# Kernel optimization log

Measured on AMD Instinct MI355X. Metric: run time of the kernel, lower is better.

## Reference

```python
import jax, jax.numpy as jnp
import numpy as np

B, K, D = 16384, 64, 128


def setup_inputs() -> dict:
    key = jax.random.key(0)
    kx, kc = jax.random.split(key)
    x = jax.random.normal(kx, (B, D), dtype=jnp.float32)
    centers = jax.random.uniform(kc, (K, D), dtype=jnp.float32)  # torch.rand init
    return {"x": x, "centers": centers}


def reference(x, centers):
    batch, dim = x.shape
    k = centers.shape[0]
    # pairwise squared distances, same math as sum((x - c)^2)
    diff = x[:, None, :] - centers[None, :, :]          # [B, K, D]
    dist_sq = jnp.sum(diff * diff, axis=-1)             # [B, K]
    expo = -0.5 * dist_sq
    # safe softmax over clusters (identical to max-subtracted exp/sum)
    resp = jax.nn.softmax(expo, axis=-1)                # [B, K]
    log_resp = jnp.log(jnp.clip(resp, 1e-8))
    # hard assignment and per-cluster statistics
    assign = jnp.argmin(dist_sq, axis=-1)               # [B] int
    onehot = jax.nn.one_hot(assign, k, dtype=x.dtype)   # [B, K]
    cluster_weight = jnp.sum(onehot, axis=0)            # [K]
    emp_total = jnp.einsum('nk,nd->kd', onehot, x)      # [K, D]
    emp_mean = emp_total / (cluster_weight[:, None] + 1e-7)
    # masked centered samples: onehot[n,k]*(x_n - mean_k) is nonzero only at k=assign(n)
    xm = x - emp_mean[assign]                           # [B, D]
    covar_total = jnp.einsum('nk,nd,ne->kde', onehot, xm, xm)  # [K, D, D]
    covar = covar_total / (cluster_weight[:, None, None] + 1e-7)
    eye = jnp.eye(dim, dtype=x.dtype)
    covar_diag = covar * eye
    covar_off = covar * (1.0 - eye)
    diag_dist_sq = jnp.sum((covar_diag - eye) ** 2, axis=(1, 2))  # [K]
    off_dist_sq = jnp.sum(covar_off ** 2, axis=(1, 2))            # [K]
    mean_dist_sq = jnp.sum((emp_mean - centers) ** 2, axis=1)     # [K]
    mean_mse = jnp.sum(cluster_weight * mean_dist_sq) / (batch * dim)
    covar_mse = jnp.sum(
        cluster_weight * diag_dist_sq / (batch * dim)
        + cluster_weight * off_dist_sq / (batch * dim * (dim - 1.0))
    )
    return log_resp, mean_mse, covar_mse
```

## Files before the change

### kernel.cpp

```cpp
#include <hip/hip_runtime.h>

#define BB 16384
#define KK 64
#define DD 128
#define SEG 128
#define MAXITEMS 192
#define NRB 4
#define RSLAB 4096
#define RBLKS (KK * NRB)

typedef __attribute__((ext_vector_type(8))) short bf16x8;
typedef __attribute__((ext_vector_type(4))) float f32x4;

__device__ __forceinline__ unsigned int packbf2(float a, float b) {
    unsigned ua = __float_as_uint(a);
    unsigned ub = __float_as_uint(b);
    ua = (ua + 0x7FFFu + ((ua >> 16) & 1u)) >> 16;
    ub = (ub + 0x7FFFu + ((ub >> 16) & 1u)) >> 16;
    return ua | (ub << 16);
}

__device__ __forceinline__ unsigned bf16rne(float f) {
    unsigned u = __float_as_uint(f);
    return (u + 0x7FFFu + ((u >> 16) & 1u)) >> 16;
}
__device__ __forceinline__ float bf16tof(unsigned h) {
    return __uint_as_float(h << 16);
}
__device__ __forceinline__ void split4(float4 v, uint2& hi, uint2& lo) {
    unsigned hx = bf16rne(v.x), hy = bf16rne(v.y);
    unsigned hz = bf16rne(v.z), hw = bf16rne(v.w);
    hi.x = hx | (hy << 16); hi.y = hz | (hw << 16);
    unsigned lx = bf16rne(v.x - bf16tof(hx)), ly = bf16rne(v.y - bf16tof(hy));
    unsigned lz = bf16rne(v.z - bf16tof(hz)), lw = bf16rne(v.w - bf16tof(hw));
    lo.x = lx | (ly << 16); lo.y = lz | (lw << 16);
}

__global__ __launch_bounds__(256) void k_rows(
    const float* __restrict__ x, const float* __restrict__ centers,
    float* __restrict__ log_resp, int* __restrict__ assign,
    int* __restrict__ bhist, int* __restrict__ counter)
{
    __shared__ unsigned int XH[64][68], XLo[64][68];
    __shared__ unsigned int CH[64][68], CLo[64][68];
    __shared__ float cn2_s[KK];
    __shared__ int   lh[KK];

    const int tid = threadIdx.x;
    const int row0 = blockIdx.x * 64;

    if (blockIdx.x == 0 && tid == 0) *counter = 0;
    if (tid < KK) lh[tid] = 0;

    for (int g = tid; g < 64 * 32; g += 256) {
        int r = g >> 5, c4g = g & 31;
        float4 v = ((const float4*)(x + (size_t)(row0 + r) * DD))[c4g];
        uint2 hi, lo; split4(v, hi, lo);
        *(uint2*)&XH[r][c4g * 2] = hi;
        *(uint2*)&XLo[r][c4g * 2] = lo;
    }
    for (int g = tid; g < 64 * 32; g += 256) {
        int k = g >> 5, c4g = g & 31;
        float4 v = ((const float4*)(centers + (size_t)k * DD))[c4g];
        uint2 hi, lo; split4(v, hi, lo);
        *(uint2*)&CH[k][c4g * 2] = hi;
        *(uint2*)&CLo[k][c4g * 2] = lo;
    }
    if (tid < KK) {
        float s = 0.f;
        const float4* cp = (const float4*)(centers + (size_t)tid * DD);
        for (int c4g = 0; c4g < 32; ++c4g) {
            float4 v = cp[c4g];
            s = fmaf(v.x, v.x, s); s = fmaf(v.y, v.y, s);
            s = fmaf(v.z, v.z, s); s = fmaf(v.w, v.w, s);
        }
        cn2_s[tid] = s;
    }
    __syncthreads();

    const int w = tid >> 6, lane = tid & 63;
    const int c4 = lane & 15, q = lane >> 4;

    f32x4 acc[4];
    #pragma unroll
    for (int nt = 0; nt < 4; ++nt) acc[nt] = (f32x4){0.f, 0.f, 0.f, 0.f};

    #pragma unroll
    for (int c = 0; c < 4; ++c) {
        const int ku = c * 16 + q * 4;
        bf16x8 ah = *(const bf16x8*)&XH[w * 16 + c4][ku];
        bf16x8 al = *(const bf16x8*)&XLo[w * 16 + c4][ku];
        #pragma unroll
        for (int nt = 0; nt < 4; ++nt) {
            bf16x8 bh = *(const bf16x8*)&CH[nt * 16 + c4][ku];
            bf16x8 bl = *(const bf16x8*)&CLo[nt * 16 + c4][ku];
            acc[nt] = __builtin_amdgcn_mfma_f32_16x16x32_bf16(ah, bh, acc[nt], 0, 0, 0);
            acc[nt] = __builtin_amdgcn_mfma_f32_16x16x32_bf16(ah, bl, acc[nt], 0, 0, 0);
            acc[nt] = __builtin_amdgcn_mfma_f32_16x16x32_bf16(al, bh, acc[nt], 0, 0, 0);
        }
    }

    float cn[4];
    #pragma unroll
    for (int nt = 0; nt < 4; ++nt) cn[nt] = 0.5f * cn2_s[nt * 16 + c4];

    #pragma unroll
    for (int j = 0; j < 4; ++j) {
        const int row = row0 + w * 16 + q * 4 + j;
        float v0 = acc[0][j] - cn[0];
        float v1 = acc[1][j] - cn[1];
        float v2 = acc[2][j] - cn[2];
        float v3 = acc[3][j] - cn[3];
        float m = v0; int idx = c4;
        if (v1 > m) { m = v1; idx = 16 + c4; }
        if (v2 > m) { m = v2; idx = 32 + c4; }
        if (v3 > m) { m = v3; idx = 48 + c4; }
        #pragma unroll
        for (int off = 1; off < 16; off <<= 1) {
            float ov = __shfl_xor(m, off);
            int   oi = __shfl_xor(idx, off);
            if (ov > m || (ov == m && oi < idx)) { m = ov; idx = oi; }
        }
        float s = expf(v0 - m) + expf(v1 - m) + expf(v2 - m) + expf(v3 - m);
        #pragma unroll
        for (int off = 1; off < 16; off <<= 1) s += __shfl_xor(s, off);
        float ls = logf(s);
        log_resp[(size_t)row * KK +  0 + c4] = fmaxf(v0 - m - ls, -18.4206807f);
        log_resp[(size_t)row * KK + 16 + c4] = fmaxf(v1 - m - ls, -18.4206807f);
        log_resp[(size_t)row * KK + 32 + c4] = fmaxf(v2 - m - ls, -18.4206807f);
        log_resp[(size_t)row * KK + 48 + c4] = fmaxf(v3 - m - ls, -18.4206807f);
        if (c4 == 0) {
            assign[row] = idx;
            atomicAdd(&lh[idx], 1);
        }
    }
    __syncthreads();
    if (tid < KK) bhist[blockIdx.x * KK + tid] = lh[tid];
}

__global__ __launch_bounds__(256) void k_scat(
    const int* __restrict__ assign, const int* __restrict__ bhist,
    int* __restrict__ sorted, float* __restrict__ cw,
    int4* __restrict__ items, int* __restrict__ item_count,
    int* __restrict__ ist, int* __restrict__ ien)
{
    __shared__ int ph_tot[4][KK], ph_pre[4][KK];
    __shared__ int cnt_s[KK], pre_s[KK], base_s[KK], cur_s[KK];
    __shared__ int iof[KK + 1];

    const int tid = threadIdx.x;
    const int b = blockIdx.x;
    const int t = tid & 63, q = tid >> 6;

    int tot = 0, pre = 0;
    const int bb0 = q * 64;
    for (int bb = bb0; bb < bb0 + 64; ++bb) {
        int v = bhist[bb * KK + t];
        tot += v;
        if (bb < b) pre += v;
    }
    ph_tot[q][t] = tot; ph_pre[q][t] = pre;
    __syncthreads();

    if (tid < KK) {
        cnt_s[tid] = ph_tot[0][tid] + ph_tot[1][tid] + ph_tot[2][tid] + ph_tot[3][tid];
        pre_s[tid] = ph_pre[0][tid] + ph_pre[1][tid] + ph_pre[2][tid] + ph_pre[3][tid];
        cur_s[tid] = 0;
    }
    __syncthreads();
    if (tid == 0) {
        int base = 0;
        for (int k = 0; k < KK; ++k) { base_s[k] = base; base += cnt_s[k]; }
    }
    __syncthreads();

    if (tid < 64) {
        int r = b * 64 + tid;
        int a = assign[r];
        int p = base_s[a] + pre_s[a] + atomicAdd(&cur_s[a], 1);
        sorted[p] = r;
    }

    if (b == 0) {
        if (tid < KK) cw[tid] = (float)cnt_s[tid];
        if (tid == 0) {
            int ic = 0;
            for (int k = 0; k < KK; ++k) {
                iof[k] = ic;
                ic += (cnt_s[k] + SEG - 1) / SEG;
            }
            iof[KK] = ic;
            *item_count = ic;
        }
        __syncthreads();
        if (tid < KK) {
            const int k = tid, c = cnt_s[k], io = iof[k];
            ist[k] = io;
            ien[k] = iof[k + 1];
            int j = 0;
            for (int s = 0; s < c; s += SEG, ++j) {
                int4 it; it.x = k; it.y = base_s[k] + s;
                it.z = min(SEG, c - s); it.w = 0;
                items[io + j] = it;
            }
        }
    }
}

__global__ __launch_bounds__(256) void k_seg(
    const float* __restrict__ x, const int* __restrict__ sorted,
    const int4* __restrict__ items, const int* __restrict__ item_count,
    float* __restrict__ part, float* __restrict__ emp_part)
{
    if ((int)blockIdx.x >= *item_count) return;
    int4 it = items[blockIdx.x];
    const int gstart = it.y, len = it.z;

    __shared__ int rows_s[128];
    __shared__ unsigned int XT[DD][68];

    const int tid = threadIdx.x;
    const int w = tid >> 6, lane = tid & 63;
    const int c4 = lane & 15, q = lane >> 4;

    f32x4 acc[2][8];
    #pragma unroll
    for (int h = 0; h < 2; ++h)
        #pragma unroll
        for (int nt = 0; nt < 8; ++nt)
            acc[h][nt] = (f32x4){0.f, 0.f, 0.f, 0.f};
    float colsum = 0.f;

    for (int half = 0; half < 2; ++half) {
        const int hoff = half * 128;
        const int hlen = min(128, len - hoff);
        if (hlen <= 0) break;

        __syncthreads();
        if (tid < hlen) rows_s[tid] = sorted[gstart + hoff + tid];
        __syncthreads();

        {
            const int r0 = 2 * lane, r1 = 2 * lane + 1;
            const int d0 = w * 32;
            const float* p0 = x + (size_t)rows_s[r0 < hlen ? r0 : 0] * DD + d0;
            const float* p1 = x + (size_t)rows_s[r1 < hlen ? r1 : 0] * DD + d0;
            #pragma unroll
            for (int i = 0; i < 8; ++i) {
                float4 a = make_float4(0.f, 0.f, 0.f, 0.f);
                float4 b = make_float4(0.f, 0.f, 0.f, 0.f);
                if (r0 < hlen) a = *(const float4*)(p0 + 4 * i);
                if (r1 < hlen) b = *(const float4*)(p1 + 4 * i);
                XT[d0 + 4 * i + 0][lane] = packbf2(a.x, b.x);
                XT[d0 + 4 * i + 1][lane] = packbf2(a.y, b.y);
                XT[d0 + 4 * i + 2][lane] = packbf2(a.z, b.z);
                XT[d0 + 4 * i + 3][lane] = packbf2(a.w, b.w);
            }
        }
        __syncthreads();

        if (tid < DD) {
            float s = 0.f;
            #pragma unroll
            for (int j4 = 0; j4 < 16; ++j4) {
                uint4 v = *(const uint4*)&XT[tid][j4 * 4];
                s += __uint_as_float(v.x << 16) + __uint_as_float(v.x & 0xFFFF0000u);
                s += __uint_as_float(v.y << 16) + __uint_as_float(v.y & 0xFFFF0000u);
                s += __uint_as_float(v.z << 16) + __uint_as_float(v.z & 0xFFFF0000u);
                s += __uint_as_float(v.w << 16) + __uint_as_float(v.w & 0xFFFF0000u);
            }
            colsum += s;
        }

        #pragma unroll
        for (int c = 0; c < 4; ++c) {
            const int ku = c * 16 + q * 4;
            bf16x8 a0 = *(const bf16x8*)&XT[(2 * w + 0) * 16 + c4][ku];
            bf16x8 a1 = *(const bf16x8*)&XT[(2 * w + 1) * 16 + c4][ku];
            #pragma unroll
            for (int nt = 0; nt < 8; ++nt) {
                bf16x8 b = *(const bf16x8*)&XT[nt * 16 + c4][ku];
                acc[0][nt] = __builtin_amdgcn_mfma_f32_16x16x32_bf16(a0, b, acc[0][nt], 0, 0, 0);
                acc[1][nt] = __builtin_amdgcn_mfma_f32_16x16x32_bf16(a1, b, acc[1][nt], 0, 0, 0);
            }
        }
    }

    if (tid < DD) emp_part[blockIdx.x * DD + tid] = colsum;

    float* pb = part + (size_t)blockIdx.x * (DD * DD);
    #pragma unroll
    for (int h = 0; h < 2; ++h) {
        const int m0 = (2 * w + h) * 16 + q * 4;
        #pragma unroll
        for (int nt = 0; nt < 8; ++nt) {
            const int n = nt * 16 + c4;
            pb[(m0 + 0) * DD + n] = acc[h][nt].x;
            pb[(m0 + 1) * DD + n] = acc[h][nt].y;
            pb[(m0 + 2) * DD + n] = acc[h][nt].z;
            pb[(m0 + 3) * DD + n] = acc[h][nt].w;
        }
    }
}

__global__ __launch_bounds__(256) void k_redfinal(
    const float* __restrict__ part, const float* __restrict__ emp_part,
    const float* __restrict__ cw, const float* __restrict__ centers,
    const int* __restrict__ ist, const int* __restrict__ ien,
    float2* __restrict__ spart, int* __restrict__ counter,
    float* __restrict__ outscalars)
{
    const int k = blockIdx.x >> 2;
    const int p = blockIdx.x & 3;
    const int i0 = ist[k], i1 = ien[k];
    const int tid = threadIdx.x;
    const int w = tid >> 6, lane = tid & 63;
    const float wgt = cw[k];
    const float inv = 1.0f / (wgt + 1e-7f);

    __shared__ float mu_s[DD], emp_s[DD];
    __shared__ float emp2[2][DD];
    __shared__ float red[4][RSLAB];

    {
        const int dh = tid & 127, hf = tid >> 7;
        float e0 = 0.f, e1 = 0.f;
        int it = i0 + hf;
        for (; it + 2 < i1; it += 4) {
            e0 += emp_part[it * DD + dh];
            e1 += emp_part[(it + 2) * DD + dh];
        }
        if (it < i1) e0 += emp_part[it * DD + dh];
        emp2[hf][dh] = e0 + e1;
    }
    __syncthreads();
    if (tid < DD) {
        float e = emp2[0][tid] + emp2[1][tid];
        emp_s[tid] = e;
        mu_s[tid] = e * inv;
    }

    float4 acc[16];
    #pragma unroll
    for (int c = 0; c < 16; ++c) acc[c] = make_float4(0.f, 0.f, 0.f, 0.f);

    const int base = p * RSLAB;
    for (int it = i0 + w; it < i1; it += 4) {
        const float* pb = part + (size_t)it * (DD * DD) + base;
        #pragma unroll
        for (int c = 0; c < 16; ++c) {
            float4 v = *(const float4*)&pb[c * 256 + lane * 4];
            acc[c].x += v.x; acc[c].y += v.y; acc[c].z += v.z; acc[c].w += v.w;
        }
    }
    #pragma unroll
    for (int c = 0; c < 16; ++c)
        *(float4*)&red[w][c * 256 + lane * 4] = acc[c];
    __syncthreads();

    float ds = 0.f, os = 0.f, mm = 0.f;
    #pragma unroll
    for (int jj = 0; jj < 16; ++jj) {
        int el = jj * 256 + tid;
        float sx = red[0][el] + red[1][el] + red[2][el] + red[3][el];
        int gel = base + el;
        int d = gel >> 7, e = gel & 127;
        float ctv = sx - mu_s[d] * emp_s[e] - emp_s[d] * mu_s[e]
                  + wgt * mu_s[d] * mu_s[e];
        float v = ctv * inv;
        if (d == e) { float t = v - 1.f; ds += t * t; }
        else        { os += v * v; }
    }
    if (p == 0 && tid < DD) {
        float t = mu_s[tid] - centers[k * DD + tid];
        mm = t * t;
    }

    #pragma unroll
    for (int off = 32; off > 0; off >>= 1) {
        ds += __shfl_down(ds, off);
        os += __shfl_down(os, off);
        mm += __shfl_down(mm, off);
    }
    __shared__ float rds[4], ros[4], rmm[4];
    __shared__ int is_last;
    if (lane == 0) { rds[w] = ds; ros[w] = os; rmm[w] = mm; }
    __syncthreads();
    if (tid == 0) {
        float DS = rds[0] + rds[1] + rds[2] + rds[3];
        float OS = ros[0] + ros[1] + ros[2] + ros[3];
        float MM = rmm[0] + rmm[1] + rmm[2] + rmm[3];
        const float bd = (float)BB * (float)DD;
        float2 mine;
        mine.x = wgt * MM / bd;
        mine.y = wgt * DS / bd + wgt * OS / (bd * (float)(DD - 1));
        spart[blockIdx.x] = mine;
        __threadfence();
        int old = atomicAdd(counter, 1);
        is_last = (old == RBLKS - 1);
    }
    __syncthreads();
    if (is_last) {
        __threadfence();
        float2 v = (tid < RBLKS) ? spart[tid] : make_float2(0.f, 0.f);
        float a = v.x, b = v.y;
        #pragma unroll
        for (int off = 32; off > 0; off >>= 1) {
            a += __shfl_down(a, off);
            b += __shfl_down(b, off);
        }
        __shared__ float ra[4], rb[4];
        if (lane == 0) { ra[w] = a; rb[w] = b; }
        __syncthreads();
        if (tid == 0) {
            outscalars[0] = ra[0] + ra[1] + ra[2] + ra[3];
            outscalars[1] = rb[0] + rb[1] + rb[2] + rb[3];
        }
    }
}

extern "C" void kernel_launch(void* const* d_in, const int* in_sizes, int n_in,
                              void* d_out, int out_size, void* d_ws, size_t ws_size,
                              hipStream_t stream) {
    const float* x = (const float*)d_in[0];
    const float* centers = (const float*)d_in[1];
    float* out = (float*)d_out;
    float* outscalars = out + (size_t)BB * KK;

    char* ws = (char*)d_ws;
    size_t off = 0;
    float*  part     = (float*)(ws + off); off += (size_t)MAXITEMS * DD * DD * 4;
    float*  emp_part = (float*)(ws + off); off += (size_t)MAXITEMS * DD * 4;
    int*    sorted   = (int*)  (ws + off); off += BB * 4;
    int*    assign   = (int*)  (ws + off); off += BB * 4;
    int*    bhist    = (int*)  (ws + off); off += 256 * KK * 4;
    int4*   items    = (int4*) (ws + off); off += 256 * 16;
    float*  cw       = (float*)(ws + off); off += 256;
    int*    itemcnt  = (int*)  (ws + off); off += 256;
    int*    ist      = (int*)  (ws + off); off += 256;
    int*    ien      = (int*)  (ws + off); off += 256;
    float2* spart    = (float2*)(ws + off); off += RBLKS * 8;
    int*    counter  = (int*)  (ws + off); off += 256;

    k_rows    <<<256, 256, 0, stream>>>(x, centers, out, assign, bhist, counter);
    k_scat    <<<256, 256, 0, stream>>>(assign, bhist, sorted, cw, items,
                                        itemcnt, ist, ien);
    k_seg     <<<MAXITEMS, 256, 0, stream>>>(x, sorted, items, itemcnt,
                                             part, emp_part);
    k_redfinal<<<RBLKS, 256, 0, stream>>>(part, emp_part, cw, centers, ist, ien,
                                          spart, counter, outscalars);
}
```

Before: 111.4 us.

## Widen segment blocks to eight waves and split reduction into more slabs

Each segment GEMM block now runs 512 threads in a single pass over its at-most-128 rows. Every wave computes one 16-row stripe of the 128x128 outer product instead of two, and the dead second half-loop is removed. The per-cluster reduction is split into 8 slabs of 2048 elements instead of 4 of 4096. That halves per-block shared memory and registers and doubles the number of reduction blocks, with the final scalar reduce adjusted to read 512 partials. The aim is more parallelism and occupancy in the two bandwidth-heavy stages, at the cost of more blocks and a little extra per-block setup.

New measurement: 115.1 us. 1.03x slower.

```diff
diff --git a/kernel.cpp b/kernel.cpp
--- a/kernel.cpp
+++ b/kernel.cpp
@@ -5,8 +5,8 @@
 #define DD 128
 #define SEG 128
 #define MAXITEMS 192
-#define NRB 4
-#define RSLAB 4096
+#define NRB 8
+#define RSLAB 2048
 #define RBLKS (KK * NRB)
 
 typedef __attribute__((ext_vector_type(8))) short bf16x8;
@@ -207,7 +207,7 @@
     }
 }
 
-__global__ __launch_bounds__(256) void k_seg(
+__global__ __launch_bounds__(512) void k_seg(
     const float* __restrict__ x, const int* __restrict__ sorted,
     const int4* __restrict__ items, const int* __restrict__ item_count,
     float* __restrict__ part, float* __restrict__ emp_part)
@@ -223,83 +223,65 @@
     const int w = tid >> 6, lane = tid & 63;
     const int c4 = lane & 15, q = lane >> 4;
 
-    f32x4 acc[2][8];
-    #pragma unroll
-    for (int h = 0; h < 2; ++h)
-        #pragma unroll
-        for (int nt = 0; nt < 8; ++nt)
-            acc[h][nt] = (f32x4){0.f, 0.f, 0.f, 0.f};
-    float colsum = 0.f;
-
-    for (int half = 0; half < 2; ++half) {
-        const int hoff = half * 128;
-        const int hlen = min(128, len - hoff);
-        if (hlen <= 0) break;
-
-        __syncthreads();
-        if (tid < hlen) rows_s[tid] = sorted[gstart + hoff + tid];
-        __syncthreads();
-
-        {
-            const int r0 = 2 * lane, r1 = 2 * lane + 1;
-            const int d0 = w * 32;
-            const float* p0 = x + (size_t)rows_s[r0 < hlen ? r0 : 0] * DD + d0;
-            const float* p1 = x + (size_t)rows_s[r1 < hlen ? r1 : 0] * DD + d0;
-            #pragma unroll
-            for (int i = 0; i < 8; ++i) {
-                float4 a = make_float4(0.f, 0.f, 0.f, 0.f);
-                float4 b = make_float4(0.f, 0.f, 0.f, 0.f);
-                if (r0 < hlen) a = *(const float4*)(p0 + 4 * i);
-                if (r1 < hlen) b = *(const float4*)(p1 + 4 * i);
-                XT[d0 + 4 * i + 0][lane] = packbf2(a.x, b.x);
-                XT[d0 + 4 * i + 1][lane] = packbf2(a.y, b.y);
-                XT[d0 + 4 * i + 2][lane] = packbf2(a.z, b.z);
-                XT[d0 + 4 * i + 3][lane] = packbf2(a.w, b.w);
-            }
-        }
-        __syncthreads();
-
-        if (tid < DD) {
-            float s = 0.f;
-            #pragma unroll
-            for (int j4 = 0; j4 < 16; ++j4) {
-                uint4 v = *(const uint4*)&XT[tid][j4 * 4];
-                s += __uint_as_float(v.x << 16) + __uint_as_float(v.x & 0xFFFF0000u);
-                s += __uint_as_float(v.y << 16) + __uint_as_float(v.y & 0xFFFF0000u);
-                s += __uint_as_float(v.z << 16) + __uint_as_float(v.z & 0xFFFF0000u);
-                s += __uint_as_float(v.w << 16) + __uint_as_float(v.w & 0xFFFF0000u);
-            }
-            colsum += s;
-        }
-
-        #pragma unroll
-        for (int c = 0; c < 4; ++c) {
-            const int ku = c * 16 + q * 4;
-            bf16x8 a0 = *(const bf16x8*)&XT[(2 * w + 0) * 16 + c4][ku];
-            bf16x8 a1 = *(const bf16x8*)&XT[(2 * w + 1) * 16 + c4][ku];
-            #pragma unroll
-            for (int nt = 0; nt < 8; ++nt) {
-                bf16x8 b = *(const bf16x8*)&XT[nt * 16 + c4][ku];
-                acc[0][nt] = __builtin_amdgcn_mfma_f32_16x16x32_bf16(a0, b, acc[0][nt], 0, 0, 0);
-                acc[1][nt] = __builtin_amdgcn_mfma_f32_16x16x32_bf16(a1, b, acc[1][nt], 0, 0, 0);
-            }
-        }
-    }
-
-    if (tid < DD) emp_part[blockIdx.x * DD + tid] = colsum;
+    f32x4 acc[8];
+    #pragma unroll
+    for (int nt = 0; nt < 8; ++nt) acc[nt] = (f32x4){0.f, 0.f, 0.f, 0.f};
+
+    if (tid < len) rows_s[tid] = sorted[gstart + tid];
+    __syncthreads();
+
+    {
+        const int r0 = 2 * lane, r1 = 2 * lane + 1;
+        const int d0 = w * 16;
+        const float* p0 = x + (size_t)rows_s[r0 < len ? r0 : 0] * DD + d0;
+        const float* p1 = x + (size_t)rows_s[r1 < len ? r1 : 0] * DD + d0;
+        #pragma unroll
+        for (int i = 0; i < 4; ++i) {
+            float4 a = make_float4(0.f, 0.f, 0.f, 0.f);
+            float4 b = make_float4(0.f, 0.f, 0.f, 0.f);
+            if (r0 < len) a = *(const float4*)(p0 + 4 * i);
+            if (r1 < len) b = *(const float4*)(p1 + 4 * i);
+            XT[d0 + 4 * i + 0][lane] = packbf2(a.x, b.x);
+            XT[d0 + 4 * i + 1][lane] = packbf2(a.y, b.y);
+            XT[d0 + 4 * i + 2][lane] = packbf2(a.z, b.z);
+            XT[d0 + 4 * i + 3][lane] = packbf2(a.w, b.w);
+        }
+    }
+    __syncthreads();
+
+    if (tid < DD) {
+        float s = 0.f;
+        #pragma unroll
+        for (int j4 = 0; j4 < 16; ++j4) {
+            uint4 v = *(const uint4*)&XT[tid][j4 * 4];
+            s += __uint_as_float(v.x << 16) + __uint_as_float(v.x & 0xFFFF0000u);
+            s += __uint_as_float(v.y << 16) + __uint_as_float(v.y & 0xFFFF0000u);
+            s += __uint_as_float(v.z << 16) + __uint_as_float(v.z & 0xFFFF0000u);
+            s += __uint_as_float(v.w << 16) + __uint_as_float(v.w & 0xFFFF0000u);
+        }
+        emp_part[blockIdx.x * DD + tid] = s;
+    }
+
+    #pragma unroll
+    for (int c = 0; c < 4; ++c) {
+        const int ku = c * 16 + q * 4;
+        bf16x8 a0 = *(const bf16x8*)&XT[w * 16 + c4][ku];
+        #pragma unroll
+        for (int nt = 0; nt < 8; ++nt) {
+            bf16x8 b = *(const bf16x8*)&XT[nt * 16 + c4][ku];
+            acc[nt] = __builtin_amdgcn_mfma_f32_16x16x32_bf16(a0, b, acc[nt], 0, 0, 0);
+        }
+    }
 
     float* pb = part + (size_t)blockIdx.x * (DD * DD);
-    #pragma unroll
-    for (int h = 0; h < 2; ++h) {
-        const int m0 = (2 * w + h) * 16 + q * 4;
-        #pragma unroll
-        for (int nt = 0; nt < 8; ++nt) {
-            const int n = nt * 16 + c4;
-            pb[(m0 + 0) * DD + n] = acc[h][nt].x;
-            pb[(m0 + 1) * DD + n] = acc[h][nt].y;
-            pb[(m0 + 2) * DD + n] = acc[h][nt].z;
-            pb[(m0 + 3) * DD + n] = acc[h][nt].w;
-        }
+    const int m0 = w * 16 + q * 4;
+    #pragma unroll
+    for (int nt = 0; nt < 8; ++nt) {
+        const int n = nt * 16 + c4;
+        pb[(m0 + 0) * DD + n] = acc[nt].x;
+        pb[(m0 + 1) * DD + n] = acc[nt].y;
+        pb[(m0 + 2) * DD + n] = acc[nt].z;
+        pb[(m0 + 3) * DD + n] = acc[nt].w;
     }
 }
 
@@ -310,8 +292,8 @@
     float2* __restrict__ spart, int* __restrict__ counter,
     float* __restrict__ outscalars)
 {
-    const int k = blockIdx.x >> 2;
-    const int p = blockIdx.x & 3;
+    const int k = blockIdx.x >> 3;
+    const int p = blockIdx.x & 7;
     const int i0 = ist[k], i1 = ien[k];
     const int tid = threadIdx.x;
     const int w = tid >> 6, lane = tid & 63;
@@ -340,27 +322,27 @@
         mu_s[tid] = e * inv;
     }
 
-    float4 acc[16];
-    #pragma unroll
-    for (int c = 0; c < 16; ++c) acc[c] = make_float4(0.f, 0.f, 0.f, 0.f);
+    float4 acc[8];
+    #pragma unroll
+    for (int c = 0; c < 8; ++c) acc[c] = make_float4(0.f, 0.f, 0.f, 0.f);
 
     const int base = p * RSLAB;
     for (int it = i0 + w; it < i1; it += 4) {
         const float* pb = part + (size_t)it * (DD * DD) + base;
         #pragma unroll
-        for (int c = 0; c < 16; ++c) {
+        for (int c = 0; c < 8; ++c) {
             float4 v = *(const float4*)&pb[c * 256 + lane * 4];
             acc[c].x += v.x; acc[c].y += v.y; acc[c].z += v.z; acc[c].w += v.w;
         }
     }
     #pragma unroll
-    for (int c = 0; c < 16; ++c)
+    for (int c = 0; c < 8; ++c)
         *(float4*)&red[w][c * 256 + lane * 4] = acc[c];
     __syncthreads();
 
     float ds = 0.f, os = 0.f, mm = 0.f;
     #pragma unroll
-    for (int jj = 0; jj < 16; ++jj) {
+    for (int jj = 0; jj < 8; ++jj) {
         int el = jj * 256 + tid;
         float sx = red[0][el] + red[1][el] + red[2][el] + red[3][el];
         int gel = base + el;
@@ -402,8 +384,9 @@
     __syncthreads();
     if (is_last) {
         __threadfence();
-        float2 v = (tid < RBLKS) ? spart[tid] : make_float2(0.f, 0.f);
-        float a = v.x, b = v.y;
+        float2 v1 = spart[tid];
+        float2 v2 = spart[tid + 256];
+        float a = v1.x + v2.x, b = v1.y + v2.y;
         #pragma unroll
         for (int off = 32; off > 0; off >>= 1) {
             a += __shfl_down(a, off);
@@ -445,7 +428,7 @@
     k_rows    <<<256, 256, 0, stream>>>(x, centers, out, assign, bhist, counter);
     k_scat    <<<256, 256, 0, stream>>>(assign, bhist, sorted, cw, items,
                                         itemcnt, ist, ien);
-    k_seg     <<<MAXITEMS, 256, 0, stream>>>(x, sorted, items, itemcnt,
+    k_seg     <<<MAXITEMS, 512, 0, stream>>>(x, sorted, items, itemcnt,
                                              part, emp_part);
     k_redfinal<<<RBLKS, 256, 0, stream>>>(part, emp_part, cw, centers, ist, ien,
                                           spart, counter, outscalars);
```
